# Kernel tuning notes

Measured on AMD Instinct MI355X. Metric: run time of the kernel, lower is better.

The kernel has to match this reference:

```python
import jax, jax.numpy as jnp
import numpy as np

B, N, C = 4, 8192, 128
NPOINT, NSAMPLE = 2048, 32
RADIUS = 0.1
EPS = 1e-5  # BatchNorm eps (eval mode with running stats)


def setup_inputs() -> dict:
    key = jax.random.key(0)
    k1, k2, k3 = jax.random.split(key, 3)
    return {
        "points_coor": jax.random.uniform(k1, (B, 3, N), dtype=jnp.float32),
        "points_fea": jax.random.normal(k2, (B, C, N), dtype=jnp.float32),
        "W": jax.random.normal(k3, (2 * C, C + 3), dtype=jnp.float32) * 0.05,
        "b": jnp.zeros((2 * C,), jnp.float32),
        "gamma": jnp.ones((2 * C,), jnp.float32),
        "beta": jnp.zeros((2 * C,), jnp.float32),
        "bn_mean": jnp.zeros((2 * C,), jnp.float32),
        "bn_var": jnp.ones((2 * C,), jnp.float32),
    }


def _fps_single(xyz):
    """Farthest point sampling for one cloud. xyz: (N,3) -> (NPOINT,) int32.
    Deterministic start at index 0 (torch version starts at a random index)."""
    n = xyz.shape[0]

    def body(carry, _):
        dist, farthest = carry
        centroid = xyz[farthest]                      # (3,)
        d = jnp.sum((xyz - centroid) ** 2, axis=-1)   # (N,)
        dist = jnp.minimum(dist, d)
        nxt = jnp.argmax(dist).astype(jnp.int32)
        return (dist, nxt), farthest

    init = (jnp.full((n,), 1e10, xyz.dtype), jnp.int32(0))
    (_, _), idx = jax.lax.scan(body, init, None, length=NPOINT)
    return idx


def _gather(points, idx):
    # points: (B,N,D), idx: (B,S,K) -> (B,S,K,D)
    return jax.vmap(lambda p, i: p[i])(points, idx)


def reference(points_coor, points_fea, W, b, gamma, beta, bn_mean, bn_var):
    coor = points_coor.transpose(0, 2, 1)  # (B,N,3)
    fea = points_fea.transpose(0, 2, 1)    # (B,N,C)

    # S: farthest point sampling
    fps_idx = jax.vmap(_fps_single)(coor)                              # (B,S)
    new_coor = jnp.take_along_axis(coor, fps_idx[:, :, None], axis=1)  # (B,S,3)

    # G: hybrid knn/ball query -- k nearest, out-of-radius replaced by nearest
    sq = (jnp.sum(new_coor ** 2, -1)[:, :, None]
          + jnp.sum(coor ** 2, -1)[:, None, :]
          - 2.0 * jnp.einsum('bsd,bnd->bsn', new_coor, coor))           # (B,S,N)
    neg_d, idx = jax.lax.top_k(-sq, NSAMPLE)                            # k smallest
    d = -neg_d
    group_idx = jnp.where(d > RADIUS ** 2, idx[:, :, 0:1], idx)         # (B,S,K)

    g_coor = (_gather(coor, group_idx) - new_coor[:, :, None, :]) / RADIUS  # (B,S,K,3)
    g_fea = _gather(fea, group_idx)                                         # (B,S,K,C)
    g = jnp.concatenate([g_fea, g_coor], axis=-1)                           # (B,S,K,C+3)

    # P: shared 1x1 conv + BN(eval) + ReLU, then max-pool over neighbors
    h = jnp.einsum('bskc,dc->bskd', g, W) + b
    h = gamma * (h - bn_mean) * jax.lax.rsqrt(bn_var + EPS) + beta
    h = jax.nn.relu(h)
    new_fea = jnp.max(h, axis=2)  # (B,S,2C)

    return new_coor.transpose(0, 2, 1), new_fea.transpose(0, 2, 1)
```

## Files before the change

kernel.cpp:

```cpp
#include <hip/hip_runtime.h>
#include <stdint.h>


typedef unsigned short u16;
typedef unsigned long long u64;
typedef __bf16 bf16x8 __attribute__((ext_vector_type(8)));
typedef float f32x4 __attribute__((ext_vector_type(4)));
typedef float f32x2 __attribute__((ext_vector_type(2)));

#define NB 4
#define NPTS 8192
#define CH 128
#define SPTS 2048
#define KN 32
#define CINP 160

__device__ __forceinline__ u16 f2b(float f) {
    unsigned x = __float_as_uint(f);
    unsigned r = (x + 0x7fffu + ((x >> 16) & 1u)) >> 16;
    return (u16)r;
}
__device__ __forceinline__ u64 umin64(u64 a, u64 b) { return a < b ? a : b; }

template <int CTRL>
__device__ __forceinline__ u64 dpp_max64(u64 k) {
    unsigned lo = (unsigned)k, hi = (unsigned)(k >> 32);
    unsigned mlo = (unsigned)__builtin_amdgcn_update_dpp((int)lo, (int)lo, CTRL, 0xF, 0xF, false);
    unsigned mhi = (unsigned)__builtin_amdgcn_update_dpp((int)hi, (int)hi, CTRL, 0xF, 0xF, false);
    u64 m = ((u64)mhi << 32) | mlo;
    return m > k ? m : k;
}
template <int CTRL>
__device__ __forceinline__ unsigned dpp_maxu(unsigned v) {
    unsigned mv = (unsigned)__builtin_amdgcn_update_dpp((int)v, (int)v, CTRL, 0xF, 0xF, false);
    return mv > v ? mv : v;
}

__global__ __launch_bounds__(256) void ktrans(const float* __restrict__ fea,
                                              u16* __restrict__ feaT) {
    __shared__ u16 T[128][130];
    int blk = blockIdx.x;
    int b = blk >> 6, nt = blk & 63;
    int n0 = nt * 128;
    int t = threadIdx.x;
#pragma unroll 4
    for (int it = 0; it < 64; ++it) {
        int idx = it * 256 + t;
        int c = idx >> 7, nl = idx & 127;
        T[nl][c] = f2b(fea[((size_t)(b * CH + c)) * NPTS + n0 + nl]);
    }
    __syncthreads();
#pragma unroll 4
    for (int it = 0; it < 64; ++it) {
        int idx = it * 256 + t;
        int nl = idx >> 7, c = idx & 127;
        feaT[((size_t)(b * NPTS + n0 + nl)) * CH + c] = T[nl][c];
    }
}

__global__ __launch_bounds__(256) void kmisc(const float* __restrict__ coor,
                                             const float* __restrict__ W,
                                             float* __restrict__ pp,
                                             u16* __restrict__ Wpad) {
    int gid = blockIdx.x * 256 + threadIdx.x;
    if (blockIdx.x < 128) {
        int n = gid & 8191, b = gid >> 13;
        const float* cb = coor + b * 3 * NPTS;
        float x = cb[n], y = cb[NPTS + n], z = cb[2 * NPTS + n];
        pp[gid] = __fadd_rn(__fadd_rn(__fmul_rn(x, x), __fmul_rn(y, y)),
                            __fmul_rn(z, z));
    } else {
        int i = gid - 128 * 256;
        if (i < 256 * CINP) {
            int d = i / CINP, k = i - d * CINP;
            Wpad[i] = (k < 131) ? f2b(W[d * 131 + k]) : (u16)0;
        }
    }
}

__global__ __launch_bounds__(256) void ksort(const float* __restrict__ coor,
                                             float* __restrict__ sxg,
                                             float* __restrict__ syg,
                                             float* __restrict__ szg,
                                             int* __restrict__ sog) {
    __shared__ int hist[256], base[256];
    int b = blockIdx.x, tid = threadIdx.x;
    const float* cb = coor + b * 3 * NPTS;
    hist[tid] = 0;
    __syncthreads();
    int bins[32];
#pragma unroll 4
    for (int i = 0; i < 32; ++i) {
        int n = tid * 32 + i;
        float x = cb[n], y = cb[NPTS + n], z = cb[2 * NPTS + n];
        int bx = min(3, (int)(x * 4.0f));
        int by = min(3, (int)(y * 4.0f));
        int bz = min(15, (int)(z * 16.0f));
        int bin = ((by * 4 + bx) << 4) | bz;
        bins[i] = bin;
        atomicAdd(&hist[bin], 1);
    }
    __syncthreads();
    if (tid == 0) {
        int acc = 0;
        for (int k2 = 0; k2 < 256; ++k2) { base[k2] = acc; acc += hist[k2]; hist[k2] = 0; }
    }
    __syncthreads();
#pragma unroll 4
    for (int i = 0; i < 32; ++i) {
        int n = tid * 32 + i;
        int bin = bins[i];
        int pos = base[bin] + atomicAdd(&hist[bin], 1);
        sxg[b * NPTS + pos] = cb[n];
        syg[b * NPTS + pos] = cb[NPTS + n];
        szg[b * NPTS + pos] = cb[2 * NPTS + n];
        sog[b * NPTS + pos] = n;
    }
}

__global__ __launch_bounds__(1024) void kfps(const float* __restrict__ sxg,
                                             const float* __restrict__ syg,
                                             const float* __restrict__ szg,
                                             const int* __restrict__ sog,
                                             int* __restrict__ fpsIdx,
                                             float* __restrict__ outCoor) {
    __shared__ float4 sp[NPTS];
    __shared__ unsigned sWin[SPTS];
    __shared__ u64 sAtom[4];
    __shared__ int slot0s;
    int tid = threadIdx.x;
    int b = blockIdx.x;
    int lane = tid & 63;
    const float* gx = sxg + b * NPTS;
    const float* gy = syg + b * NPTS;
    const float* gz = szg + b * NPTS;
    const int* go = sog + b * NPTS;
    f32x2 X2[4], Y2[4], Z2[4], D2[4];
    unsigned PK[8];
    int n0 = tid * 8;
    if (tid < 4) sAtom[tid] = 0;
    float lox, hix, loy, hiy, loz, hiz;
#pragma unroll
    for (int j = 0; j < 8; ++j) {
        float x = gx[n0 + j], y = gy[n0 + j], z = gz[n0 + j];
        sp[n0 + j] = make_float4(x, y, z, 0.0f);
        X2[j >> 1][j & 1] = x; Y2[j >> 1][j & 1] = y; Z2[j >> 1][j & 1] = z;
        D2[j >> 1][j & 1] = 1e10f;
        int oi = go[n0 + j];
        PK[j] = ((unsigned)oi << 16) | (unsigned)(n0 + j);
        if (oi == 0) slot0s = n0 + j;
        if (j == 0) {
            lox = hix = x; loy = hiy = y; loz = hiz = z;
        } else {
            lox = fminf(lox, x); hix = fmaxf(hix, x);
            loy = fminf(loy, y); hiy = fmaxf(hiy, y);
            loz = fminf(loz, z); hiz = fmaxf(hiz, z);
        }
    }
    __syncthreads();
    int far = slot0s;
    if (tid == 0) sWin[0] = (unsigned)slot0s;
    float lm = 3.4e38f;
    u64 cachedKey = 1;
    for (int t = 1; t < SPTS; ++t) {
        float4 c = sp[far];
        float fx = c.x, fy = c.y, fz = c.z;
        float ddx = fmaxf(0.0f, fmaxf(lox - fx, fx - hix));
        float ddy = fmaxf(0.0f, fmaxf(loy - fy, fy - hiy));
        float ddz = fmaxf(0.0f, fmaxf(loz - fz, fz - hiz));
        float dmin2 = ddx * ddx + ddy * ddy + ddz * ddz;
        if (__ballot(dmin2 * 0.9995f < lm) != 0ull) {
            {
#pragma clang fp contract(off)
                f32x2 fx2 = {fx, fx}, fy2 = {fy, fy}, fz2 = {fz, fz};
#pragma unroll
                for (int i = 0; i < 4; ++i) {
                    f32x2 dx = X2[i] - fx2;
                    f32x2 dy = Y2[i] - fy2;
                    f32x2 dz = Z2[i] - fz2;
                    f32x2 s = (dx * dx + dy * dy) + dz * dz;
                    D2[i] = __builtin_elementwise_min(D2[i], s);
                }
            }
            f32x2 t01 = __builtin_elementwise_max(D2[0], D2[1]);
            f32x2 t23 = __builtin_elementwise_max(D2[2], D2[3]);
            f32x2 t03 = __builtin_elementwise_max(t01, t23);
            float m = fmaxf(t03[0], t03[1]);
            lm = m;
            unsigned sel = 0xFFFFFFFFu;
#pragma unroll
            for (int j = 0; j < 8; ++j) {
                float dj = D2[j >> 1][j & 1];
                sel = (dj == m) ? (sel < PK[j] ? sel : PK[j]) : sel;
            }
            unsigned mbits = __float_as_uint(m);
            unsigned r = mbits;
            r = dpp_maxu<0xB1>(r);
            r = dpp_maxu<0x4E>(r);
            r = dpp_maxu<0x141>(r);
            r = dpp_maxu<0x140>(r);
            r = dpp_maxu<0x142>(r);
            r = dpp_maxu<0x143>(r);
            unsigned wmaxb = (unsigned)__builtin_amdgcn_readlane((int)r, 63);
            u64 ball = __ballot(mbits == wmaxb);
            unsigned wpk;
            if (__popcll(ball) == 1) {
                int l = __ffsll(ball) - 1;
                wpk = (unsigned)__builtin_amdgcn_readlane((int)sel, l);
            } else {
                u64 kk = (mbits == wmaxb) ? (((u64)wmaxb << 32) | (unsigned)~sel) : 0ull;
                kk = dpp_max64<0xB1>(kk);
                kk = dpp_max64<0x4E>(kk);
                kk = dpp_max64<0x141>(kk);
                kk = dpp_max64<0x140>(kk);
                kk = dpp_max64<0x142>(kk);
                kk = dpp_max64<0x143>(kk);
                unsigned lo = (unsigned)__builtin_amdgcn_readlane((int)(unsigned)kk, 63);
                wpk = ~lo;
            }
            cachedKey = ((u64)wmaxb << 32) | (unsigned)~wpk;
        }
        if (lane == 63) atomicMax(&sAtom[t & 3], cachedKey);
        if (tid == 0) sAtom[(t + 1) & 3] = 0;
        __syncthreads();
        u64 wk = sAtom[t & 3];
        unsigned pk = ~(unsigned)wk;
        far = (int)(pk & 0xFFFFu);
        if (tid == 0) sWin[t] = pk;
    }
    __syncthreads();
    for (int i = tid; i < SPTS; i += 1024) {
        unsigned pk = sWin[i];
        int slot = (int)(pk & 0xFFFFu);
        float4 c = sp[slot];
        fpsIdx[b * SPTS + i] = (int)(pk >> 16);
        float* oc = outCoor + b * 3 * SPTS + i;
        oc[0] = c.x; oc[SPTS] = c.y; oc[2 * SPTS] = c.z;
    }
}

__global__ __launch_bounds__(256) void kgroup(const float* __restrict__ coor,
                                              const float* __restrict__ pp,
                                              const int* __restrict__ fpsIdx,
                                              int* __restrict__ gidxOut) {
    __shared__ u64 buf[4][256];
    __shared__ int cnt[4];
    int tid = threadIdx.x;
    int wv = tid >> 6, lane = tid & 63;
    if (tid < 4) cnt[tid] = 0;
    __syncthreads();
    int row = blockIdx.x * 4 + wv;
    int b = row >> 11, s = row & 2047;
    const float* cb = coor + b * 3 * NPTS;
    int n0 = fpsIdx[b * SPTS + s];
    float cx = cb[n0], cy = cb[NPTS + n0], cz = cb[2 * NPTS + n0];
    float cc = __fadd_rn(__fadd_rn(__fmul_rn(cx, cx), __fmul_rn(cy, cy)),
                         __fmul_rn(cz, cz));
    const float* ppb = pp + b * NPTS;
    u64 mk = ~0ull;
    for (int n = lane; n < NPTS; n += 64) {
        float x = cb[n], y = cb[NPTS + n], z = cb[2 * NPTS + n];
        float dot = __fmaf_rn(cz, z, __fmaf_rn(cy, y, __fmul_rn(cx, x)));
        float sq = __fsub_rn(__fadd_rn(cc, ppb[n]), __fmul_rn(2.0f, dot));
        unsigned ub = __float_as_uint(sq);
        ub ^= (ub >> 31) ? 0xFFFFFFFFu : 0x80000000u;
        u64 key = ((u64)ub << 32) | (unsigned)n;
        mk = umin64(mk, key);
        if (sq <= 0.01f) {
            int p = atomicAdd(&cnt[wv], 1);
            if (p < 256) buf[wv][p] = key;
        }
    }
#pragma unroll
    for (int off = 32; off > 0; off >>= 1) mk = umin64(mk, __shfl_xor(mk, off));
    int C = cnt[wv];
    if (C > 256) C = 256;
    int* go = gidxOut + row * KN;
    if (C <= 32) {
        if (lane < 32) {
            unsigned idx = (lane < C) ? (unsigned)buf[wv][lane] : (unsigned)mk;
            go[lane] = (int)idx;
        }
    } else {
        u64 e[4];
#pragma unroll
        for (int i = 0; i < 4; ++i) {
            int j2 = lane + (i << 6);
            e[i] = (j2 < C) ? buf[wv][j2] : ~0ull;
        }
        int cl = 0;
        unsigned sel = 0;
        for (int it = 0; it < 32; ++it) {
            u64 lb = ~0ull;
            int li = 0;
#pragma unroll
            for (int i = 0; i < 4; ++i) {
                bool f = (((cl >> i) & 1) == 0) && (e[i] < lb);
                lb = f ? e[i] : lb;
                li = f ? i : li;
            }
            u64 wmin = lb;
#pragma unroll
            for (int off = 32; off > 0; off >>= 1) wmin = umin64(wmin, __shfl_xor(wmin, off));
            u64 bal = __ballot(lb == wmin);
            int src = __ffsll((unsigned long long)bal) - 1;
            if (lane == src) cl |= (1 << li);
            if (lane == it) sel = (unsigned)wmin;
        }
        if (lane < 32) go[lane] = (int)sel;
    }
}

__global__ __launch_bounds__(256) void kfeat(const float* __restrict__ coor,
                                             const u16* __restrict__ feaT,
                                             const u16* __restrict__ Wpad,
                                             const float* __restrict__ bias,
                                             const float* __restrict__ gamma,
                                             const float* __restrict__ beta,
                                             const float* __restrict__ bmean,
                                             const float* __restrict__ bvar,
                                             const int* __restrict__ fpsIdx,
                                             const int* __restrict__ gidx,
                                             float* __restrict__ outFea) {
    __shared__ u16 g[KN][168];
    int row = blockIdx.x;
    int b = row >> 11, s = row & 2047;
    int tid = threadIdx.x;
    {
        int k = tid >> 3, j = tid & 7;
        const float* cb = coor + b * 3 * NPTS;
        int nc = fpsIdx[b * SPTS + s];
        int nbr = gidx[row * KN + k];
        const uint4* f4 = (const uint4*)(feaT + (((size_t)b * NPTS + nbr) << 7));
        uint4* gr = (uint4*)&g[k][0];
        gr[j] = f4[j];
        gr[j + 8] = f4[j + 8];
        for (int c = 128 + j; c < CINP; c += 8) {
            u16 v = 0;
            if (c < 131) {
                int dim = c - 128;
                float pv = cb[dim * NPTS + nbr];
                float cv = cb[dim * NPTS + nc];
                v = f2b(__fdiv_rn(__fsub_rn(pv, cv), 0.1f));
            }
            g[k][c] = v;
        }
    }
    __syncthreads();
    int w = tid >> 6, lane = tid & 63;
    int mrow = lane & 15, q = lane >> 4;
    f32x4 acc[4][2] = {};
#pragma unroll
    for (int ks = 0; ks < 5; ++ks) {
        int kb = ks * 32 + q * 8;
        bf16x8 b0 = *(const bf16x8*)&g[mrow][kb];
        bf16x8 b1 = *(const bf16x8*)&g[mrow + 16][kb];
#pragma unroll
        for (int mt = 0; mt < 4; ++mt) {
            bf16x8 a = *(const bf16x8*)&Wpad[(size_t)(w * 64 + mt * 16 + mrow) * CINP + kb];
            acc[mt][0] = __builtin_amdgcn_mfma_f32_16x16x32_bf16(a, b0, acc[mt][0], 0, 0, 0);
            acc[mt][1] = __builtin_amdgcn_mfma_f32_16x16x32_bf16(a, b1, acc[mt][1], 0, 0, 0);
        }
    }
#pragma unroll
    for (int mt = 0; mt < 4; ++mt) {
#pragma unroll
        for (int r = 0; r < 4; ++r) {
            int m = w * 64 + mt * 16 + q * 4 + r;
            float ga = gamma[m], be = beta[m];
            float mu = bmean[m], va = bvar[m], bi = bias[m];
            float rs = 1.0f / sqrtf(va + 1e-5f);
            float h0 = acc[mt][0][r] + bi;
            h0 = fmaxf(ga * (h0 - mu) * rs + be, 0.0f);
            float h1 = acc[mt][1][r] + bi;
            h1 = fmaxf(ga * (h1 - mu) * rs + be, 0.0f);
            float v = fmaxf(h0, h1);
#pragma unroll
            for (int off = 1; off < 16; off <<= 1) v = fmaxf(v, __shfl_xor(v, off));
            if (mrow == 0) outFea[((size_t)(b * 256 + m)) * SPTS + s] = v;
        }
    }
}

extern "C" void kernel_launch(void* const* d_in, const int* in_sizes, int n_in,
                              void* d_out, int out_size, void* d_ws, size_t ws_size,
                              hipStream_t stream) {
    const float* coor = (const float*)d_in[0];
    const float* fea = (const float*)d_in[1];
    const float* W = (const float*)d_in[2];
    const float* bias = (const float*)d_in[3];
    const float* gamma = (const float*)d_in[4];
    const float* beta = (const float*)d_in[5];
    const float* bmean = (const float*)d_in[6];
    const float* bvar = (const float*)d_in[7];
    char* ws = (char*)d_ws;
    int* fpsIdx = (int*)ws;
    int* gidx = (int*)(ws + 32768);
    float* pp = (float*)(ws + 32768 + 1048576);
    u16* feaT = (u16*)(ws + 1212416);
    u16* Wpad = (u16*)(ws + 9601024);
    float* sxg = (float*)(ws + 9682944);
    float* syg = (float*)(ws + 9814016);
    float* szg = (float*)(ws + 9945088);
    int* sog = (int*)(ws + 10076160);
    float* outC = (float*)d_out;
    float* outF = outC + NB * 3 * SPTS;

    ktrans<<<256, 256, 0, stream>>>(fea, feaT);
    kmisc<<<288, 256, 0, stream>>>(coor, W, pp, Wpad);
    ksort<<<NB, 256, 0, stream>>>(coor, sxg, syg, szg, sog);
    kfps<<<NB, 1024, 0, stream>>>(sxg, syg, szg, sog, fpsIdx, outC);
    kgroup<<<2048, 256, 0, stream>>>(coor, pp, fpsIdx, gidx);
    kfeat<<<8192, 256, 0, stream>>>(coor, feaT, Wpad, bias, gamma, beta, bmean, bvar,
                                    fpsIdx, gidx, outF);
}
```

Baseline: 1.647 ms.

## Fuse prep kernels and skip FPS wave reduction when wave winner persists

Merges the transpose, misc and sort kernels into one launch, so the three small prep kernels run as a single grid. In the FPS loop each wave now remembers its previous winning point and tracks how far it is from new centroids. When that point's distance still equals the wave's stored maximum, the per-wave DPP argmax reduction is skipped and the cached key is reused. The box-distance test is also rewritten in centre/half-extent form. This adds branch and register overhead and needs careful handling of tie cases to stay correct.

```diff
diff --git a/kernel.cpp b/kernel.cpp
--- a/kernel.cpp
+++ b/kernel.cpp
@@ -36,85 +36,86 @@
     return mv > v ? mv : v;
 }
 
-__global__ __launch_bounds__(256) void ktrans(const float* __restrict__ fea,
-                                              u16* __restrict__ feaT) {
-    __shared__ u16 T[128][130];
-    int blk = blockIdx.x;
-    int b = blk >> 6, nt = blk & 63;
-    int n0 = nt * 128;
-    int t = threadIdx.x;
-#pragma unroll 4
-    for (int it = 0; it < 64; ++it) {
-        int idx = it * 256 + t;
-        int c = idx >> 7, nl = idx & 127;
-        T[nl][c] = f2b(fea[((size_t)(b * CH + c)) * NPTS + n0 + nl]);
-    }
-    __syncthreads();
-#pragma unroll 4
-    for (int it = 0; it < 64; ++it) {
-        int idx = it * 256 + t;
-        int nl = idx >> 7, c = idx & 127;
-        feaT[((size_t)(b * NPTS + n0 + nl)) * CH + c] = T[nl][c];
-    }
-}
-
-__global__ __launch_bounds__(256) void kmisc(const float* __restrict__ coor,
+__global__ __launch_bounds__(256) void kprep(const float* __restrict__ fea,
+                                             const float* __restrict__ coor,
                                              const float* __restrict__ W,
+                                             u16* __restrict__ feaT,
                                              float* __restrict__ pp,
-                                             u16* __restrict__ Wpad) {
-    int gid = blockIdx.x * 256 + threadIdx.x;
-    if (blockIdx.x < 128) {
-        int n = gid & 8191, b = gid >> 13;
-        const float* cb = coor + b * 3 * NPTS;
-        float x = cb[n], y = cb[NPTS + n], z = cb[2 * NPTS + n];
-        pp[gid] = __fadd_rn(__fadd_rn(__fmul_rn(x, x), __fmul_rn(y, y)),
-                            __fmul_rn(z, z));
-    } else {
-        int i = gid - 128 * 256;
-        if (i < 256 * CINP) {
-            int d = i / CINP, k = i - d * CINP;
-            Wpad[i] = (k < 131) ? f2b(W[d * 131 + k]) : (u16)0;
-        }
-    }
-}
-
-__global__ __launch_bounds__(256) void ksort(const float* __restrict__ coor,
+                                             u16* __restrict__ Wpad,
                                              float* __restrict__ sxg,
                                              float* __restrict__ syg,
                                              float* __restrict__ szg,
                                              int* __restrict__ sog) {
-    __shared__ int hist[256], base[256];
-    int b = blockIdx.x, tid = threadIdx.x;
-    const float* cb = coor + b * 3 * NPTS;
-    hist[tid] = 0;
-    __syncthreads();
-    int bins[32];
+    __shared__ __align__(16) char raw[128 * 130 * 2];
+    int bid = blockIdx.x;
+    int t = threadIdx.x;
+    if (bid < 256) {
+        u16(*T)[130] = (u16(*)[130])raw;
+        int b = bid >> 6, nt = bid & 63;
+        int n0 = nt * 128;
 #pragma unroll 4
-    for (int i = 0; i < 32; ++i) {
-        int n = tid * 32 + i;
-        float x = cb[n], y = cb[NPTS + n], z = cb[2 * NPTS + n];
-        int bx = min(3, (int)(x * 4.0f));
-        int by = min(3, (int)(y * 4.0f));
-        int bz = min(15, (int)(z * 16.0f));
-        int bin = ((by * 4 + bx) << 4) | bz;
-        bins[i] = bin;
-        atomicAdd(&hist[bin], 1);
-    }
-    __syncthreads();
-    if (tid == 0) {
-        int acc = 0;
-        for (int k2 = 0; k2 < 256; ++k2) { base[k2] = acc; acc += hist[k2]; hist[k2] = 0; }
-    }
-    __syncthreads();
+        for (int it = 0; it < 64; ++it) {
+            int idx = it * 256 + t;
+            int c = idx >> 7, nl = idx & 127;
+            T[nl][c] = f2b(fea[((size_t)(b * CH + c)) * NPTS + n0 + nl]);
+        }
+        __syncthreads();
 #pragma unroll 4
-    for (int i = 0; i < 32; ++i) {
-        int n = tid * 32 + i;
-        int bin = bins[i];
-        int pos = base[bin] + atomicAdd(&hist[bin], 1);
-        sxg[b * NPTS + pos] = cb[n];
-        syg[b * NPTS + pos] = cb[NPTS + n];
-        szg[b * NPTS + pos] = cb[2 * NPTS + n];
-        sog[b * NPTS + pos] = n;
+        for (int it = 0; it < 64; ++it) {
+            int idx = it * 256 + t;
+            int nl = idx >> 7, c = idx & 127;
+            feaT[((size_t)(b * NPTS + n0 + nl)) * CH + c] = T[nl][c];
+        }
+    } else if (bid < 544) {
+        int gid = (bid - 256) * 256 + t;
+        if (bid < 384) {
+            int n = gid & 8191, b = gid >> 13;
+            const float* cb = coor + b * 3 * NPTS;
+            float x = cb[n], y = cb[NPTS + n], z = cb[2 * NPTS + n];
+            pp[gid] = __fadd_rn(__fadd_rn(__fmul_rn(x, x), __fmul_rn(y, y)),
+                                __fmul_rn(z, z));
+        } else {
+            int i = gid - 128 * 256;
+            if (i < 256 * CINP) {
+                int d = i / CINP, k = i - d * CINP;
+                Wpad[i] = (k < 131) ? f2b(W[d * 131 + k]) : (u16)0;
+            }
+        }
+    } else {
+        int* hist = (int*)raw;
+        int* base = hist + 256;
+        int b = bid - 544;
+        const float* cb = coor + b * 3 * NPTS;
+        hist[t] = 0;
+        __syncthreads();
+        int bins[32];
+#pragma unroll 4
+        for (int i = 0; i < 32; ++i) {
+            int n = t * 32 + i;
+            float x = cb[n], y = cb[NPTS + n], z = cb[2 * NPTS + n];
+            int bx = min(3, (int)(x * 4.0f));
+            int by = min(3, (int)(y * 4.0f));
+            int bz = min(15, (int)(z * 16.0f));
+            int bin = ((by * 4 + bx) << 4) | bz;
+            bins[i] = bin;
+            atomicAdd(&hist[bin], 1);
+        }
+        __syncthreads();
+        if (t == 0) {
+            int acc = 0;
+            for (int k2 = 0; k2 < 256; ++k2) { base[k2] = acc; acc += hist[k2]; hist[k2] = 0; }
+        }
+        __syncthreads();
+#pragma unroll 4
+        for (int i = 0; i < 32; ++i) {
+            int n = t * 32 + i;
+            int bin = bins[i];
+            int pos = base[bin] + atomicAdd(&hist[bin], 1);
+            sxg[b * NPTS + pos] = cb[n];
+            syg[b * NPTS + pos] = cb[NPTS + n];
+            szg[b * NPTS + pos] = cb[2 * NPTS + n];
+            sog[b * NPTS + pos] = n;
+        }
     }
 }
 
@@ -157,19 +158,27 @@
             loz = fminf(loz, z); hiz = fmaxf(hiz, z);
         }
     }
+    float bcx = (lox + hix) * 0.5f, bex = (hix - lox) * 0.5f;
+    float bcy = (loy + hiy) * 0.5f, bey = (hiy - loy) * 0.5f;
+    float bcz = (loz + hiz) * 0.5f, bez = (hiz - loz) * 0.5f;
     __syncthreads();
     int far = slot0s;
     if (tid == 0) sWin[0] = (unsigned)slot0s;
     float lm = 3.4e38f;
+    float wMaxF = 3.4e38f;
     u64 cachedKey = 1;
+    bool win = false;
+    float bX = 0.f, bY = 0.f, bZ = 0.f;
+    float cvD = 3.4e38f;
     for (int t = 1; t < SPTS; ++t) {
         float4 c = sp[far];
         float fx = c.x, fy = c.y, fz = c.z;
-        float ddx = fmaxf(0.0f, fmaxf(lox - fx, fx - hix));
-        float ddy = fmaxf(0.0f, fmaxf(loy - fy, fy - hiy));
-        float ddz = fmaxf(0.0f, fmaxf(loz - fz, fz - hiz));
+        float ddx = fmaxf(0.0f, fabsf(fx - bcx) - bex);
+        float ddy = fmaxf(0.0f, fabsf(fy - bcy) - bey);
+        float ddz = fmaxf(0.0f, fabsf(fz - bcz) - bez);
         float dmin2 = ddx * ddx + ddy * ddy + ddz * ddz;
         if (__ballot(dmin2 * 0.9995f < lm) != 0ull) {
+            float sc;
             {
 #pragma clang fp contract(off)
                 f32x2 fx2 = {fx, fx}, fy2 = {fy, fy}, fz2 = {fz, fz};
@@ -181,44 +190,65 @@
                     f32x2 s = (dx * dx + dy * dy) + dz * dz;
                     D2[i] = __builtin_elementwise_min(D2[i], s);
                 }
+                float cdx = bX - fx, cdy = bY - fy, cdz = bZ - fz;
+                sc = (cdx * cdx + cdy * cdy) + cdz * cdz;
             }
+            cvD = fminf(cvD, sc);
             f32x2 t01 = __builtin_elementwise_max(D2[0], D2[1]);
             f32x2 t23 = __builtin_elementwise_max(D2[2], D2[3]);
             f32x2 t03 = __builtin_elementwise_max(t01, t23);
             float m = fmaxf(t03[0], t03[1]);
             lm = m;
-            unsigned sel = 0xFFFFFFFFu;
-#pragma unroll
-            for (int j = 0; j < 8; ++j) {
-                float dj = D2[j >> 1][j & 1];
-                sel = (dj == m) ? (sel < PK[j] ? sel : PK[j]) : sel;
+            if (__ballot(win && (cvD == wMaxF)) == 0ull) {
+                unsigned sel = 0xFFFFFFFFu;
+#pragma unroll
+                for (int j = 0; j < 8; ++j) {
+                    float dj = D2[j >> 1][j & 1];
+                    sel = (dj == m) ? (sel < PK[j] ? sel : PK[j]) : sel;
+                }
+                unsigned mbits = __float_as_uint(m);
+                unsigned r = mbits;
+                r = dpp_maxu<0xB1>(r);
+                r = dpp_maxu<0x4E>(r);
+                r = dpp_maxu<0x141>(r);
+                r = dpp_maxu<0x140>(r);
+                r = dpp_maxu<0x142>(r);
+                r = dpp_maxu<0x143>(r);
+                unsigned wmaxb = (unsigned)__builtin_amdgcn_readlane((int)r, 63);
+                u64 ball = __ballot(mbits == wmaxb);
+                unsigned wpk;
+                bool iw;
+                if (__popcll(ball) == 1) {
+                    int l = __ffsll(ball) - 1;
+                    wpk = (unsigned)__builtin_amdgcn_readlane((int)sel, l);
+                    iw = (mbits == wmaxb);
+                } else {
+                    u64 kk = (mbits == wmaxb) ? (((u64)wmaxb << 32) | (unsigned)~sel) : 0ull;
+                    kk = dpp_max64<0xB1>(kk);
+                    kk = dpp_max64<0x4E>(kk);
+                    kk = dpp_max64<0x141>(kk);
+                    kk = dpp_max64<0x140>(kk);
+                    kk = dpp_max64<0x142>(kk);
+                    kk = dpp_max64<0x143>(kk);
+                    unsigned lo = (unsigned)__builtin_amdgcn_readlane((int)(unsigned)kk, 63);
+                    wpk = ~lo;
+                    iw = (mbits == wmaxb) && ((unsigned)~sel == lo);
+                }
+                win = iw;
+                if (iw) {
+                    cvD = m;
+#pragma unroll
+                    for (int j = 0; j < 8; ++j) {
+                        if (PK[j] == sel) {
+                            bX = X2[j >> 1][j & 1];
+                            bY = Y2[j >> 1][j & 1];
+                            bZ = Z2[j >> 1][j & 1];
+                        }
+                    }
+                }
+                cachedKey = ((u64)wmaxb << 32) | (unsigned)~wpk;
+                wMaxF = __uint_as_float(wmaxb);
             }
-            unsigned mbits = __float_as_uint(m);
-            unsigned r = mbits;
-            r = dpp_maxu<0xB1>(r);
-            r = dpp_maxu<0x4E>(r);
-            r = dpp_maxu<0x141>(r);
-            r = dpp_maxu<0x140>(r);
-            r = dpp_maxu<0x142>(r);
-            r = dpp_maxu<0x143>(r);
-            unsigned wmaxb = (unsigned)__builtin_amdgcn_readlane((int)r, 63);
-            u64 ball = __ballot(mbits == wmaxb);
-            unsigned wpk;
-            if (__popcll(ball) == 1) {
-                int l = __ffsll(ball) - 1;
-                wpk = (unsigned)__builtin_amdgcn_readlane((int)sel, l);
-            } else {
-                u64 kk = (mbits == wmaxb) ? (((u64)wmaxb << 32) | (unsigned)~sel) : 0ull;
-                kk = dpp_max64<0xB1>(kk);
-                kk = dpp_max64<0x4E>(kk);
-                kk = dpp_max64<0x141>(kk);
-                kk = dpp_max64<0x140>(kk);
-                kk = dpp_max64<0x142>(kk);
-                kk = dpp_max64<0x143>(kk);
-                unsigned lo = (unsigned)__builtin_amdgcn_readlane((int)(unsigned)kk, 63);
-                wpk = ~lo;
-            }
-            cachedKey = ((u64)wmaxb << 32) | (unsigned)~wpk;
         }
         if (lane == 63) atomicMax(&sAtom[t & 3], cachedKey);
         if (tid == 0) sAtom[(t + 1) & 3] = 0;
@@ -406,9 +436,7 @@
     float* outC = (float*)d_out;
     float* outF = outC + NB * 3 * SPTS;
 
-    ktrans<<<256, 256, 0, stream>>>(fea, feaT);
-    kmisc<<<288, 256, 0, stream>>>(coor, W, pp, Wpad);
-    ksort<<<NB, 256, 0, stream>>>(coor, sxg, syg, szg, sog);
+    kprep<<<548, 256, 0, stream>>>(fea, coor, W, feaT, pp, Wpad, sxg, syg, szg, sog);
     kfps<<<NB, 1024, 0, stream>>>(sxg, syg, szg, sog, fpsIdx, outC);
     kgroup<<<2048, 256, 0, stream>>>(coor, pp, fpsIdx, gidx);
     kfeat<<<8192, 256, 0, stream>>>(coor, feaT, Wpad, bias, gamma, beta, bmean, bvar,
```

New measurement: 1.764 ms. 7.1% more time.

## Fold transpose and misc prep into extra FPS blocks to overlap with sampling

Applied to the files above, without the earlier changes.

Removes the separate transpose and misc kernels and runs their work in extra blocks of the FPS launch (blocks 4..139), so it executes on otherwise idle CUs while the four serial FPS blocks run. This takes two launches and their serialized time off the critical path. The cost is that the transpose now uses 1024-thread blocks reusing the FPS shared buffer, and the FPS kernel's large shared-memory footprint may limit how many helper blocks co-reside per CU.

```diff
diff --git a/kernel.cpp b/kernel.cpp
--- a/kernel.cpp
+++ b/kernel.cpp
@@ -34,48 +34,6 @@
 __device__ __forceinline__ unsigned dpp_maxu(unsigned v) {
     unsigned mv = (unsigned)__builtin_amdgcn_update_dpp((int)v, (int)v, CTRL, 0xF, 0xF, false);
     return mv > v ? mv : v;
-}
-
-__global__ __launch_bounds__(256) void ktrans(const float* __restrict__ fea,
-                                              u16* __restrict__ feaT) {
-    __shared__ u16 T[128][130];
-    int blk = blockIdx.x;
-    int b = blk >> 6, nt = blk & 63;
-    int n0 = nt * 128;
-    int t = threadIdx.x;
-#pragma unroll 4
-    for (int it = 0; it < 64; ++it) {
-        int idx = it * 256 + t;
-        int c = idx >> 7, nl = idx & 127;
-        T[nl][c] = f2b(fea[((size_t)(b * CH + c)) * NPTS + n0 + nl]);
-    }
-    __syncthreads();
-#pragma unroll 4
-    for (int it = 0; it < 64; ++it) {
-        int idx = it * 256 + t;
-        int nl = idx >> 7, c = idx & 127;
-        feaT[((size_t)(b * NPTS + n0 + nl)) * CH + c] = T[nl][c];
-    }
-}
-
-__global__ __launch_bounds__(256) void kmisc(const float* __restrict__ coor,
-                                             const float* __restrict__ W,
-                                             float* __restrict__ pp,
-                                             u16* __restrict__ Wpad) {
-    int gid = blockIdx.x * 256 + threadIdx.x;
-    if (blockIdx.x < 128) {
-        int n = gid & 8191, b = gid >> 13;
-        const float* cb = coor + b * 3 * NPTS;
-        float x = cb[n], y = cb[NPTS + n], z = cb[2 * NPTS + n];
-        pp[gid] = __fadd_rn(__fadd_rn(__fmul_rn(x, x), __fmul_rn(y, y)),
-                            __fmul_rn(z, z));
-    } else {
-        int i = gid - 128 * 256;
-        if (i < 256 * CINP) {
-            int d = i / CINP, k = i - d * CINP;
-            Wpad[i] = (k < 131) ? f2b(W[d * 131 + k]) : (u16)0;
-        }
-    }
 }
 
 __global__ __launch_bounds__(256) void ksort(const float* __restrict__ coor,
@@ -123,13 +81,58 @@
                                              const float* __restrict__ szg,
                                              const int* __restrict__ sog,
                                              int* __restrict__ fpsIdx,
-                                             float* __restrict__ outCoor) {
+                                             float* __restrict__ outCoor,
+                                             const float* __restrict__ fea,
+                                             const float* __restrict__ coor,
+                                             const float* __restrict__ W,
+                                             u16* __restrict__ feaT,
+                                             float* __restrict__ pp,
+                                             u16* __restrict__ Wpad) {
     __shared__ float4 sp[NPTS];
     __shared__ unsigned sWin[SPTS];
     __shared__ u64 sAtom[4];
     __shared__ int slot0s;
+    int bid = blockIdx.x;
     int tid = threadIdx.x;
-    int b = blockIdx.x;
+    if (bid >= 4) {
+        if (bid < 68) {
+            u16(*T)[130] = (u16(*)[130])sp;
+            int base_t = (bid - 4) * 4;
+#pragma unroll 1
+            for (int k = 0; k < 4; ++k) {
+                int tidx = base_t + k;
+                int b = tidx >> 6, nt = tidx & 63;
+                int n0 = nt * 128;
+#pragma unroll 4
+                for (int it = 0; it < 16; ++it) {
+                    int idx = it * 1024 + tid;
+                    int c = idx >> 7, nl = idx & 127;
+                    T[nl][c] = f2b(fea[((size_t)(b * CH + c)) * NPTS + n0 + nl]);
+                }
+                __syncthreads();
+#pragma unroll 4
+                for (int it = 0; it < 16; ++it) {
+                    int idx = it * 1024 + tid;
+                    int nl = idx >> 7, c = idx & 127;
+                    feaT[((size_t)(b * NPTS + n0 + nl)) * CH + c] = T[nl][c];
+                }
+                __syncthreads();
+            }
+        } else if (bid < 100) {
+            int gid = (bid - 68) * 1024 + tid;
+            int n = gid & 8191, b = gid >> 13;
+            const float* cb = coor + b * 3 * NPTS;
+            float x = cb[n], y = cb[NPTS + n], z = cb[2 * NPTS + n];
+            pp[gid] = __fadd_rn(__fadd_rn(__fmul_rn(x, x), __fmul_rn(y, y)),
+                                __fmul_rn(z, z));
+        } else {
+            int i = (bid - 100) * 1024 + tid;
+            int d = i / CINP, k = i - d * CINP;
+            Wpad[i] = (k < 131) ? f2b(W[d * 131 + k]) : (u16)0;
+        }
+        return;
+    }
+    int b = bid;
     int lane = tid & 63;
     const float* gx = sxg + b * NPTS;
     const float* gy = syg + b * NPTS;
@@ -406,10 +409,9 @@
     float* outC = (float*)d_out;
     float* outF = outC + NB * 3 * SPTS;
 
-    ktrans<<<256, 256, 0, stream>>>(fea, feaT);
-    kmisc<<<288, 256, 0, stream>>>(coor, W, pp, Wpad);
     ksort<<<NB, 256, 0, stream>>>(coor, sxg, syg, szg, sog);
-    kfps<<<NB, 1024, 0, stream>>>(sxg, syg, szg, sog, fpsIdx, outC);
+    kfps<<<140, 1024, 0, stream>>>(sxg, syg, szg, sog, fpsIdx, outC,
+                                   fea, coor, W, feaT, pp, Wpad);
     kgroup<<<2048, 256, 0, stream>>>(coor, pp, fpsIdx, gidx);
     kfeat<<<8192, 256, 0, stream>>>(coor, feaT, Wpad, bias, gamma, beta, bmean, bvar,
                                     fpsIdx, gidx, outF);
```

Result: no change. 1.664 ms (+1.0%).
